# Performance work log

Hardware: AMD Instinct MI355X
Metric: run time of the kernel (lower is better)

## Reference

```python
import jax, jax.numpy as jnp
import numpy as np

B, N, D_MODEL, H, DK, DV = 2, 2048, 512, 8, 64, 64


def setup_inputs() -> dict:
    key = jax.random.key(0)
    ks = jax.random.split(key, 15)
    s = 0.02
    f = jnp.float32
    inp = {
        "x": jax.random.normal(ks[0], (B, N, D_MODEL), f),
        # frozen base projections
        "Wq": jax.random.normal(ks[1], (D_MODEL, H * DK), f) * s,
        "bq": jax.random.normal(ks[2], (H * DK,), f) * s,
        "Wk": jax.random.normal(ks[3], (D_MODEL, H * DK), f) * s,
        "bk": jax.random.normal(ks[4], (H * DK,), f) * s,
        "Wv": jax.random.normal(ks[5], (D_MODEL, H * DV), f) * s,
        "bv": jax.random.normal(ks[6], (H * DV,), f) * s,
        # 'lora' adapters (full linears in the source, added to base)
        "Wq_lora": jax.random.normal(ks[7], (D_MODEL, H * DK), f) * s,
        "bq_lora": jax.random.normal(ks[8], (H * DK,), f) * s,
        "Wk_lora": jax.random.normal(ks[9], (D_MODEL, H * DK), f) * s,
        "bk_lora": jax.random.normal(ks[10], (H * DK,), f) * s,
        "Wv_lora": jax.random.normal(ks[11], (D_MODEL, H * DV), f) * s,
        "bv_lora": jax.random.normal(ks[12], (H * DV,), f) * s,
        # output projection
        "Wo": jax.random.normal(ks[13], (H * DV, D_MODEL), f) * s,
        "bo": jax.random.normal(ks[14], (D_MODEL,), f) * s,
    }
    return inp


def reference(x, Wq, bq, Wk, bk, Wv, bv,
              Wq_lora, bq_lora, Wk_lora, bk_lora, Wv_lora, bv_lora,
              Wo, bo):
    b, n, _ = x.shape
    # base + lora pairs share the same input -> fuse into single GEMMs
    q = x @ (Wq + Wq_lora) + (bq + bq_lora)          # [b, n, H*DK]
    k = x @ (Wk + Wk_lora) + (bk + bk_lora)          # [b, n, H*DK]
    v = x @ (Wv + Wv_lora) + (bv + bv_lora)          # [b, n, H*DV]

    q = q.reshape(b, n, H, DK).transpose(0, 2, 1, 3)  # [b, H, n, DK]
    k = k.reshape(b, n, H, DK).transpose(0, 2, 1, 3)
    v = v.reshape(b, n, H, DV).transpose(0, 2, 1, 3)

    scale = 1.0 / jnp.sqrt(jnp.asarray(DK, x.dtype))
    scores = jnp.einsum('bhqd,bhkd->bhqk', q, k) * scale  # [b, H, n, n]
    att = jax.nn.softmax(scores, axis=-1)                 # attn dropout = eval identity
    out = jnp.einsum('bhqk,bhkd->bhqd', att, v)           # [b, H, n, DV]
    out = out.transpose(0, 2, 1, 3).reshape(b, n, H * DV)
    return out @ Wo + bo                                  # resid dropout = eval identity
```

## Files before the change

kernel.cpp:

```cpp
#include <hip/hip_runtime.h>
#include <hip/hip_bf16.h>

#define B_  2
#define N_  2048
#define DM_ 512
#define H_  8
#define DK_ 64
#define DV_ 64
#define BN_ (B_*N_)
#define SPLITS 2

typedef __attribute__((ext_vector_type(8))) short short8;
typedef __attribute__((ext_vector_type(4))) float f32x4;
typedef unsigned short ushort;

static __device__ __forceinline__ ushort f2bf(float x) {
    unsigned int u = __float_as_uint(x);
    unsigned int r = (u + 0x7FFFu + ((u >> 16) & 1u)) >> 16;
    return (ushort)r;
}
static __device__ __forceinline__ float bf2f(ushort u) {
    return __uint_as_float(((unsigned)u) << 16);
}
static __device__ __forceinline__ float exp2_fast(float x) {
    float r; asm("v_exp_f32 %0, %1" : "=v"(r) : "v"(x)); return r;
}
static __device__ __forceinline__ unsigned cvt_pk_bf16(float a, float b) {
    unsigned r; asm("v_cvt_pk_bf16_f32 %0, %1, %2" : "=v"(r) : "v"(a), "v"(b)); return r;
}

#define LOG2E 1.4426950408889634f

__global__ __launch_bounds__(256) void fuse_transpose4(
        const float* __restrict__ W0, const float* __restrict__ L0,
        const float* __restrict__ W1, const float* __restrict__ L1,
        const float* __restrict__ W2, const float* __restrict__ L2,
        const float* __restrict__ W3, ushort* __restrict__ WtBase) {
    const int z = blockIdx.z;
    const float* W  = (z == 0) ? W0 : (z == 1) ? W1 : (z == 2) ? W2 : W3;
    const float* WL = (z == 0) ? L0 : (z == 1) ? L1 : (z == 2) ? L2 : nullptr;
    ushort* Wt = WtBase + (size_t)z * DM_ * DM_;

    __shared__ float Ws[32][65];
    const int t  = threadIdx.x;
    const int c0 = blockIdx.x * 64;
    const int k0 = blockIdx.y * 32;
    {
        int r = t >> 4, cq = t & 15;
#pragma unroll
        for (int it = 0; it < 2; ++it) {
            int rr = r + it * 16;
            float4 v = *reinterpret_cast<const float4*>(W + (size_t)(k0 + rr) * DM_ + c0 + cq * 4);
            if (WL) {
                float4 u = *reinterpret_cast<const float4*>(WL + (size_t)(k0 + rr) * DM_ + c0 + cq * 4);
                v.x += u.x; v.y += u.y; v.z += u.z; v.w += u.w;
            }
            Ws[rr][cq * 4 + 0] = v.x; Ws[rr][cq * 4 + 1] = v.y;
            Ws[rr][cq * 4 + 2] = v.z; Ws[rr][cq * 4 + 3] = v.w;
        }
    }
    __syncthreads();
    {
        int cr = t >> 2, kq = t & 3;
        short8 o;
#pragma unroll
        for (int j = 0; j < 8; ++j) o[j] = (short)f2bf(Ws[kq * 8 + j][cr]);
        *reinterpret_cast<short8*>(Wt + (size_t)(c0 + cr) * DM_ + k0 + kq * 8) = o;
    }
}

__global__ void fuse_bias(const float* __restrict__ bq, const float* __restrict__ bqL,
                          const float* __restrict__ bk, const float* __restrict__ bkL,
                          const float* __restrict__ bv, const float* __restrict__ bvL,
                          float* __restrict__ fb) {
    int idx = blockIdx.x * blockDim.x + threadIdx.x;
    if (idx >= 3 * DM_) return;
    int w = idx >> 9, i = idx & 511;
    const float* a = (w == 0) ? bq : (w == 1) ? bk : bv;
    const float* b = (w == 0) ? bqL : (w == 1) ? bkL : bvL;
    fb[idx] = a[i] + b[i];
}

__global__ void xcast(const float* __restrict__ x, ushort* __restrict__ xb) {
    size_t idx = (size_t)blockIdx.x * blockDim.x + threadIdx.x;
    float4 v0 = *reinterpret_cast<const float4*>(x + idx * 8);
    float4 v1 = *reinterpret_cast<const float4*>(x + idx * 8 + 4);
    short8 o;
    o[0] = (short)f2bf(v0.x); o[1] = (short)f2bf(v0.y);
    o[2] = (short)f2bf(v0.z); o[3] = (short)f2bf(v0.w);
    o[4] = (short)f2bf(v1.x); o[5] = (short)f2bf(v1.y);
    o[6] = (short)f2bf(v1.z); o[7] = (short)f2bf(v1.w);
    *reinterpret_cast<short8*>(xb + idx * 8) = o;
}

template<int BN, int MODE>
__global__ __launch_bounds__(256) void gemm_bf16(const ushort* __restrict__ A,
                                                 const ushort* __restrict__ Bt,
                                                 const float* __restrict__ bias,
                                                 ushort* __restrict__ Qd,
                                                 ushort* __restrict__ Kd,
                                                 ushort* __restrict__ Vd,
                                                 float* __restrict__ outF) {
    constexpr int NWC = BN / 64;
    constexpr int NWR = 4 / NWC;
    constexpr int MI  = (128 / NWR) / 16;
    constexpr int NJ  = 4;
    const int rt = blockIdx.x, ct = blockIdx.y;
    __shared__ ushort As[128 * 64];
    __shared__ ushort Bs[BN * 64];
    const int t = threadIdx.x, lane = t & 63, w = t >> 6;
    const int wr = w / NWC, wc = w % NWC;
    const int lg = lane >> 4, lr = lane & 15;
    const int rowbase = wr * (128 / NWR);
    const int colbase = wc * 64;

    f32x4 acc[MI][NJ];
#pragma unroll
    for (int mi = 0; mi < MI; ++mi)
#pragma unroll
        for (int nj = 0; nj < NJ; ++nj) acc[mi][nj] = (f32x4){0.f, 0.f, 0.f, 0.f};

    for (int k0 = 0; k0 < DM_; k0 += 64) {
        __syncthreads();
#pragma unroll
        for (int it = 0; it < 4; ++it) {
            int cid = t + it * 256;
            int r = cid >> 3, cq = cid & 7;
            uint4 vld = *reinterpret_cast<const uint4*>(
                A + ((size_t)(rt * 128 + r)) * DM_ + k0 + cq * 8);
            *reinterpret_cast<uint4*>((char*)As + r * 128 + ((cq ^ (r & 7)) << 4)) = vld;
        }
#pragma unroll
        for (int it = 0; it < BN * 8 / 256; ++it) {
            int cid = t + it * 256;
            int r = cid >> 3, cq = cid & 7;
            uint4 vld = *reinterpret_cast<const uint4*>(
                Bt + ((size_t)(ct * BN + r)) * DM_ + k0 + cq * 8);
            *reinterpret_cast<uint4*>((char*)Bs + r * 128 + ((cq ^ (r & 7)) << 4)) = vld;
        }
        __syncthreads();
#pragma unroll
        for (int kh = 0; kh < 2; ++kh) {
            short8 a[MI], b[NJ];
#pragma unroll
            for (int mi = 0; mi < MI; ++mi) {
                int row = rowbase + mi * 16 + lr;
                a[mi] = *reinterpret_cast<const short8*>(
                    (char*)As + row * 128 + (((kh * 4 + lg) ^ (row & 7)) << 4));
            }
#pragma unroll
            for (int nj = 0; nj < NJ; ++nj) {
                int row = colbase + nj * 16 + lr;
                b[nj] = *reinterpret_cast<const short8*>(
                    (char*)Bs + row * 128 + (((kh * 4 + lg) ^ (row & 7)) << 4));
            }
#pragma unroll
            for (int mi = 0; mi < MI; ++mi)
#pragma unroll
                for (int nj = 0; nj < NJ; ++nj)
                    acc[mi][nj] = __builtin_amdgcn_mfma_f32_16x16x32_bf16(
                        a[mi], b[nj], acc[mi][nj], 0, 0, 0);
        }
    }

#pragma unroll
    for (int mi = 0; mi < MI; ++mi) {
#pragma unroll
        for (int nj = 0; nj < NJ; ++nj) {
#pragma unroll
            for (int r = 0; r < 4; ++r) {
                int m = rt * 128 + rowbase + mi * 16 + 4 * lg + r;
                int n = ct * BN + colbase + nj * 16 + lr;
                float v = acc[mi][nj][r] + bias[n];
                if (MODE == 0) {
                    int ws_ = n >> 9;
                    if (ws_ == 0) v *= 0.125f * LOG2E;
                    ushort* op = (ws_ == 0) ? Qd : (ws_ == 1) ? Kd : Vd;
                    int hd = (n >> 6) & 7, d = n & 63;
                    int bb = m >> 11, nn = m & (N_ - 1);
                    op[(((size_t)(bb * H_ + hd)) * N_ + nn) * DK_ + d] = f2bf(v);
                } else {
                    outF[(size_t)m * DM_ + n] = v;
                }
            }
        }
    }
}

__global__ __launch_bounds__(256) void vtrans(const ushort* __restrict__ Vd,
                                              ushort* __restrict__ Vt) {
    const int bh = blockIdx.y, nt = blockIdx.x;
    __shared__ ushort Ls[64 * 64];
    char* LB = (char*)Ls;
    const int t = threadIdx.x;
#pragma unroll
    for (int i = 0; i < 2; ++i) {
        int c = t + i * 256;
        int tok = c >> 3, dc = c & 7;
        uint4 v = *reinterpret_cast<const uint4*>(
            Vd + ((size_t)bh * N_ + nt * 64 + tok) * DV_ + dc * 8);
        int sw = dc ^ (tok & 7) ^ ((tok >> 3) & 7);
        *reinterpret_cast<uint4*>(LB + tok * 128 + (sw << 4)) = v;
    }
    __syncthreads();
#pragma unroll
    for (int i = 0; i < 2; ++i) {
        int c = t + i * 256;
        int d = c >> 3, tc = c & 7;
        short8 g;
#pragma unroll
        for (int j = 0; j < 8; ++j) {
            int tok = tc * 8 + j;
            int sw = (d >> 3) ^ (tok & 7) ^ ((tok >> 3) & 7);
            g[j] = *reinterpret_cast<const ushort*>(LB + tok * 128 + (sw << 4) + (d & 7) * 2);
        }
        *reinterpret_cast<short8*>(Vt + ((size_t)bh * DV_ + d) * N_ + nt * 64 + tc * 8) = g;
    }
}

__global__ __launch_bounds__(512) void attn_mfma(const ushort* __restrict__ Q,
                                                 const ushort* __restrict__ K,
                                                 const ushort* __restrict__ Vt,
                                                 ushort* __restrict__ Opart,
                                                 float2* __restrict__ Ml) {
    const int bh = blockIdx.y;
    const int qt = blockIdx.x;
    const int sp = blockIdx.z;
    const int t  = threadIdx.x;
    const int lane = t & 63;
    const int w  = t >> 6;
    const int lg = lane >> 4;
    const int lr = lane & 15;

    __shared__ ushort KsBuf[2][64 * 64];
    __shared__ ushort VtBuf[2][64 * 64];
    __shared__ ushort Ps[8][16 * 64];
    char* PsB = (char*)(Ps[w]);

    const ushort* Kb  = K  + ((size_t)bh * N_ + sp * (N_ / 2)) * DK_;
    const ushort* Vtb = Vt + (size_t)bh * DV_ * N_ + sp * (N_ / 2);

    const int srow = t >> 3, sc = t & 7;

    short8 qf[2];
    {
        const ushort* qrow = Q + ((size_t)bh * N_ + qt * 128 + w * 16 + lr) * DK_;
        qf[0] = *reinterpret_cast<const short8*>(qrow + 8 * lg);
        qf[1] = *reinterpret_cast<const short8*>(qrow + 32 + 8 * lg);
    }

    f32x4 o_[4];
#pragma unroll
    for (int i = 0; i < 4; i++) o_[i] = (f32x4){0.f, 0.f, 0.f, 0.f};
    float m1 = -1e30f, l1 = 0.f;

    uint4 kreg, vreg;
    auto issue = [&](int kt_) {
        kreg = *reinterpret_cast<const uint4*>(Kb  + ((size_t)(kt_ * 64 + srow)) * DK_ + sc * 8);
        vreg = *reinterpret_cast<const uint4*>(Vtb + (size_t)srow * N_ + kt_ * 64 + sc * 8);
    };
    auto wstage = [&](int buf_) {
        *reinterpret_cast<uint4*>((char*)(KsBuf[buf_]) + srow * 128 + ((sc ^ (srow & 7)) << 4)) = kreg;
        *reinterpret_cast<uint4*>((char*)(VtBuf[buf_]) + srow * 128 + ((sc ^ (srow & 7)) << 4)) = vreg;
    };

    issue(0);
    wstage(0);
    __syncthreads();

    const int NT = (N_ / 2) / 64;
    for (int kt = 0; kt < NT; ++kt) {
        const int cur = kt & 1;
        if (kt + 1 < NT) issue(kt + 1);

        char* KsB = (char*)(KsBuf[cur]);
        char* VtB = (char*)(VtBuf[cur]);

        f32x4 s[4];
#pragma unroll
        for (int kb = 0; kb < 4; ++kb) {
            int row = kb * 16 + lr;
            short8 k0 = *reinterpret_cast<const short8*>(
                KsB + row * 128 + ((lg ^ (row & 7)) << 4));
            short8 k1 = *reinterpret_cast<const short8*>(
                KsB + row * 128 + (((4 + lg) ^ (row & 7)) << 4));
            f32x4 z = (f32x4){0.f, 0.f, 0.f, 0.f};
            s[kb] = __builtin_amdgcn_mfma_f32_16x16x32_bf16(k0, qf[0], z, 0, 0, 0);
            s[kb] = __builtin_amdgcn_mfma_f32_16x16x32_bf16(k1, qf[1], s[kb], 0, 0, 0);
        }

        float mx = s[0][0];
#pragma unroll
        for (int kb = 0; kb < 4; ++kb)
#pragma unroll
            for (int r = 0; r < 4; ++r) mx = fmaxf(mx, s[kb][r]);
        mx = fmaxf(mx, __shfl_xor(mx, 16));
        mx = fmaxf(mx, __shfl_xor(mx, 32));

        if (!__all(mx <= m1 + 8.0f)) {
            float mnew = fmaxf(m1, mx);
            float alpha = exp2_fast(m1 - mnew);
            m1 = mnew;
            l1 *= alpha;
#pragma unroll
            for (int r = 0; r < 4; ++r) {
                float ar = __shfl(alpha, 4 * lg + r);
#pragma unroll
                for (int db = 0; db < 4; ++db) o_[db][r] *= ar;
            }
        }

        float p[4][4];
        float sum = 0.f;
#pragma unroll
        for (int kb = 0; kb < 4; ++kb)
#pragma unroll
            for (int r = 0; r < 4; ++r) { p[kb][r] = exp2_fast(s[kb][r] - m1); sum += p[kb][r]; }
        sum += __shfl_xor(sum, 16);
        sum += __shfl_xor(sum, 32);
        l1 += sum;

#pragma unroll
        for (int kb = 0; kb < 4; ++kb) {
            uint2 pk;
            pk.x = cvt_pk_bf16(p[kb][0], p[kb][1]);
            pk.y = cvt_pk_bf16(p[kb][2], p[kb][3]);
            int chunk = 2 * kb + (lg >> 1);
            *reinterpret_cast<uint2*>(
                PsB + lr * 128 + ((chunk ^ (lr & 7)) << 4) + (lg & 1) * 8) = pk;
        }

        short8 pf[2];
        {
            pf[0] = *reinterpret_cast<const short8*>(
                PsB + lr * 128 + ((lg ^ (lr & 7)) << 4));
            pf[1] = *reinterpret_cast<const short8*>(
                PsB + lr * 128 + (((4 + lg) ^ (lr & 7)) << 4));
        }
#pragma unroll
        for (int db = 0; db < 4; ++db) {
            int row = db * 16 + lr;
            short8 v0 = *reinterpret_cast<const short8*>(
                VtB + row * 128 + ((lg ^ (row & 7)) << 4));
            short8 v1 = *reinterpret_cast<const short8*>(
                VtB + row * 128 + (((4 + lg) ^ (row & 7)) << 4));
            o_[db] = __builtin_amdgcn_mfma_f32_16x16x32_bf16(pf[0], v0, o_[db], 0, 0, 0);
            o_[db] = __builtin_amdgcn_mfma_f32_16x16x32_bf16(pf[1], v1, o_[db], 0, 0, 0);
        }

        if (kt + 1 < NT) wstage(cur ^ 1);
        __syncthreads();
    }

    const size_t rowbase = ((size_t)(sp * 16 + bh)) * N_ + qt * 128 + w * 16;
#pragma unroll
    for (int r = 0; r < 4; ++r) {
        int n_loc = 4 * lg + r;
#pragma unroll
        for (int db = 0; db < 4; ++db) {
            Opart[(rowbase + n_loc) * DV_ + db * 16 + lr] = f2bf(o_[db][r]);
        }
    }
    if (lg == 0) {
        Ml[rowbase + lr] = make_float2(m1, l1);
    }
}

__global__ __launch_bounds__(256) void merge_splits(const ushort* __restrict__ Opart,
                                                    const float2* __restrict__ Ml,
                                                    ushort* __restrict__ Od) {
    int gid = blockIdx.x * 256 + threadIdx.x;
    int row = gid >> 4;
    int dv  = (gid & 15) * 4;
    const int R = 16 * N_;
    float2 ml0 = Ml[row];
    float2 ml1 = Ml[R + row];
    float M  = fmaxf(ml0.x, ml1.x);
    float w0 = exp2_fast(ml0.x - M);
    float w1 = exp2_fast(ml1.x - M);
    float inv = 1.f / (w0 * ml0.y + w1 * ml1.y);
    uint2 a = *reinterpret_cast<const uint2*>(Opart + (size_t)row * DV_ + dv);
    uint2 b = *reinterpret_cast<const uint2*>(Opart + ((size_t)R + row) * DV_ + dv);
    const ushort* ae = reinterpret_cast<const ushort*>(&a);
    const ushort* be = reinterpret_cast<const ushort*>(&b);
    uint2 o;
    unsigned* oe = reinterpret_cast<unsigned*>(&o);
#pragma unroll
    for (int half = 0; half < 2; ++half) {
        float v0 = (w0 * bf2f(ae[half * 2 + 0]) + w1 * bf2f(be[half * 2 + 0])) * inv;
        float v1 = (w0 * bf2f(ae[half * 2 + 1]) + w1 * bf2f(be[half * 2 + 1])) * inv;
        oe[half] = cvt_pk_bf16(v0, v1);
    }
    int bh = row >> 11, n = row & (N_ - 1);
    int bb = bh >> 3, h = bh & 7;
    *reinterpret_cast<uint2*>(Od + ((size_t)(bb * N_ + n)) * (H_ * DV_) + h * DV_ + dv) = o;
}

extern "C" void kernel_launch(void* const* d_in, const int* in_sizes, int n_in,
                              void* d_out, int out_size, void* d_ws, size_t ws_size,
                              hipStream_t stream) {
    const float* x   = (const float*)d_in[0];
    const float* Wq  = (const float*)d_in[1];
    const float* bq  = (const float*)d_in[2];
    const float* Wk  = (const float*)d_in[3];
    const float* bk  = (const float*)d_in[4];
    const float* Wv  = (const float*)d_in[5];
    const float* bv  = (const float*)d_in[6];
    const float* WqL = (const float*)d_in[7];
    const float* bqL = (const float*)d_in[8];
    const float* WkL = (const float*)d_in[9];
    const float* bkL = (const float*)d_in[10];
    const float* WvL = (const float*)d_in[11];
    const float* bvL = (const float*)d_in[12];
    const float* Wo  = (const float*)d_in[13];
    const float* bo  = (const float*)d_in[14];

    ushort* Wt_all = (ushort*)d_ws;
    ushort* Wot    = Wt_all + (size_t)3 * DM_ * DM_;
    float*  fb     = (float*)(Wt_all + (size_t)4 * DM_ * DM_);
    ushort* xbf    = (ushort*)(fb + 3 * DM_);
    ushort* Qd     = xbf + (size_t)BN_ * DM_;
    ushort* Kd     = Qd + (size_t)B_ * H_ * N_ * DK_;
    ushort* Vd     = Kd + (size_t)B_ * H_ * N_ * DK_;
    ushort* Vtd    = Vd + (size_t)B_ * H_ * N_ * DV_;
    ushort* Od     = Vtd + (size_t)B_ * H_ * N_ * DV_;
    ushort* Opart  = Od + (size_t)B_ * H_ * N_ * DV_;
    float2* Ml     = (float2*)(Opart + (size_t)SPLITS * B_ * H_ * N_ * DV_);

    float* out = (float*)d_out;

    fuse_transpose4<<<dim3(8, 16, 4), 256, 0, stream>>>(Wq, WqL, Wk, WkL, Wv, WvL, Wo, Wt_all);
    fuse_bias<<<6, 256, 0, stream>>>(bq, bqL, bk, bkL, bv, bvL, fb);
    xcast<<<1024, 256, 0, stream>>>(x, xbf);

    gemm_bf16<128, 0><<<dim3(32, 12), 256, 0, stream>>>(xbf, Wt_all, fb, Qd, Kd, Vd, nullptr);
    vtrans<<<dim3(32, 16), 256, 0, stream>>>(Vd, Vtd);
    attn_mfma<<<dim3(16, 16, SPLITS), 512, 0, stream>>>(Qd, Kd, Vtd, Opart, Ml);
    merge_splits<<<(B_ * H_ * N_ * 16) / 256, 256, 0, stream>>>(Opart, Ml, Od);
    gemm_bf16<64, 1><<<dim3(32, 8), 256, 0, stream>>>(Od, Wot, bo, nullptr, nullptr, nullptr, out);
}
```

Before: 72.08 us.

## Double-buffer GEMM shared-memory staging and merge xcast with bias fusion

The bf16 GEMM now prefetches the next K-tile from global memory into registers while running the MFMAs on the current tile, then writes it into a second LDS buffer. This cuts one barrier per iteration and hides global load latency. The cost is doubled LDS use and extra registers, which may lower occupancy. Separately, the x cast and the bias fusion now run in one kernel, saving a launch.

New measurement: 103.6 us. 1.44x slower.

```diff
diff --git a/kernel.cpp b/kernel.cpp
--- a/kernel.cpp
+++ b/kernel.cpp
@@ -69,28 +69,31 @@
     }
 }
 
-__global__ void fuse_bias(const float* __restrict__ bq, const float* __restrict__ bqL,
-                          const float* __restrict__ bk, const float* __restrict__ bkL,
-                          const float* __restrict__ bv, const float* __restrict__ bvL,
-                          float* __restrict__ fb) {
-    int idx = blockIdx.x * blockDim.x + threadIdx.x;
-    if (idx >= 3 * DM_) return;
-    int w = idx >> 9, i = idx & 511;
-    const float* a = (w == 0) ? bq : (w == 1) ? bk : bv;
-    const float* b = (w == 0) ? bqL : (w == 1) ? bkL : bvL;
-    fb[idx] = a[i] + b[i];
-}
-
-__global__ void xcast(const float* __restrict__ x, ushort* __restrict__ xb) {
-    size_t idx = (size_t)blockIdx.x * blockDim.x + threadIdx.x;
-    float4 v0 = *reinterpret_cast<const float4*>(x + idx * 8);
-    float4 v1 = *reinterpret_cast<const float4*>(x + idx * 8 + 4);
-    short8 o;
-    o[0] = (short)f2bf(v0.x); o[1] = (short)f2bf(v0.y);
-    o[2] = (short)f2bf(v0.z); o[3] = (short)f2bf(v0.w);
-    o[4] = (short)f2bf(v1.x); o[5] = (short)f2bf(v1.y);
-    o[6] = (short)f2bf(v1.z); o[7] = (short)f2bf(v1.w);
-    *reinterpret_cast<short8*>(xb + idx * 8) = o;
+__global__ void xcast_bias(const float* __restrict__ x, ushort* __restrict__ xb,
+                           const float* __restrict__ bq, const float* __restrict__ bqL,
+                           const float* __restrict__ bk, const float* __restrict__ bkL,
+                           const float* __restrict__ bv, const float* __restrict__ bvL,
+                           float* __restrict__ fb) {
+    const int bid = blockIdx.x;
+    if (bid < 1024) {
+        size_t idx = (size_t)bid * blockDim.x + threadIdx.x;
+        float4 v0 = *reinterpret_cast<const float4*>(x + idx * 8);
+        float4 v1 = *reinterpret_cast<const float4*>(x + idx * 8 + 4);
+        short8 o;
+        o[0] = (short)f2bf(v0.x); o[1] = (short)f2bf(v0.y);
+        o[2] = (short)f2bf(v0.z); o[3] = (short)f2bf(v0.w);
+        o[4] = (short)f2bf(v1.x); o[5] = (short)f2bf(v1.y);
+        o[6] = (short)f2bf(v1.z); o[7] = (short)f2bf(v1.w);
+        *reinterpret_cast<short8*>(xb + idx * 8) = o;
+    } else {
+        int idx = (bid - 1024) * 256 + threadIdx.x;
+        if (idx < 3 * DM_) {
+            int w = idx >> 9, i = idx & 511;
+            const float* a = (w == 0) ? bq : (w == 1) ? bk : bv;
+            const float* b = (w == 0) ? bqL : (w == 1) ? bkL : bvL;
+            fb[idx] = a[i] + b[i];
+        }
+    }
 }
 
 template<int BN, int MODE>
@@ -105,14 +108,16 @@
     constexpr int NWR = 4 / NWC;
     constexpr int MI  = (128 / NWR) / 16;
     constexpr int NJ  = 4;
+    constexpr int BIT = BN * 8 / 256;
     const int rt = blockIdx.x, ct = blockIdx.y;
-    __shared__ ushort As[128 * 64];
-    __shared__ ushort Bs[BN * 64];
+    __shared__ ushort As[2][128 * 64];
+    __shared__ ushort Bs[2][BN * 64];
     const int t = threadIdx.x, lane = t & 63, w = t >> 6;
     const int wr = w / NWC, wc = w % NWC;
     const int lg = lane >> 4, lr = lane & 15;
     const int rowbase = wr * (128 / NWR);
     const int colbase = wc * 64;
+    const int sr = t >> 3, scq = t & 7;
 
     f32x4 acc[MI][NJ];
 #pragma unroll
@@ -120,25 +125,43 @@
 #pragma unroll
         for (int nj = 0; nj < NJ; ++nj) acc[mi][nj] = (f32x4){0.f, 0.f, 0.f, 0.f};
 
+    uint4 aReg[4], bReg[BIT];
+    auto issue = [&](int k0) {
+#pragma unroll
+        for (int it = 0; it < 4; ++it) {
+            int r = sr + it * 32;
+            aReg[it] = *reinterpret_cast<const uint4*>(
+                A + ((size_t)(rt * 128 + r)) * DM_ + k0 + scq * 8);
+        }
+#pragma unroll
+        for (int it = 0; it < BIT; ++it) {
+            int r = sr + it * 32;
+            bReg[it] = *reinterpret_cast<const uint4*>(
+                Bt + ((size_t)(ct * BN + r)) * DM_ + k0 + scq * 8);
+        }
+    };
+    auto wstage = [&](int buf) {
+#pragma unroll
+        for (int it = 0; it < 4; ++it) {
+            int r = sr + it * 32;
+            *reinterpret_cast<uint4*>(
+                (char*)(As[buf]) + r * 128 + ((scq ^ (r & 7)) << 4)) = aReg[it];
+        }
+#pragma unroll
+        for (int it = 0; it < BIT; ++it) {
+            int r = sr + it * 32;
+            *reinterpret_cast<uint4*>(
+                (char*)(Bs[buf]) + r * 128 + ((scq ^ (r & 7)) << 4)) = bReg[it];
+        }
+    };
+
+    issue(0);
+    wstage(0);
+    __syncthreads();
+
     for (int k0 = 0; k0 < DM_; k0 += 64) {
-        __syncthreads();
-#pragma unroll
-        for (int it = 0; it < 4; ++it) {
-            int cid = t + it * 256;
-            int r = cid >> 3, cq = cid & 7;
-            uint4 vld = *reinterpret_cast<const uint4*>(
-                A + ((size_t)(rt * 128 + r)) * DM_ + k0 + cq * 8);
-            *reinterpret_cast<uint4*>((char*)As + r * 128 + ((cq ^ (r & 7)) << 4)) = vld;
-        }
-#pragma unroll
-        for (int it = 0; it < BN * 8 / 256; ++it) {
-            int cid = t + it * 256;
-            int r = cid >> 3, cq = cid & 7;
-            uint4 vld = *reinterpret_cast<const uint4*>(
-                Bt + ((size_t)(ct * BN + r)) * DM_ + k0 + cq * 8);
-            *reinterpret_cast<uint4*>((char*)Bs + r * 128 + ((cq ^ (r & 7)) << 4)) = vld;
-        }
-        __syncthreads();
+        const int cur = (k0 >> 6) & 1;
+        if (k0 + 64 < DM_) issue(k0 + 64);
 #pragma unroll
         for (int kh = 0; kh < 2; ++kh) {
             short8 a[MI], b[NJ];
@@ -146,13 +169,13 @@
             for (int mi = 0; mi < MI; ++mi) {
                 int row = rowbase + mi * 16 + lr;
                 a[mi] = *reinterpret_cast<const short8*>(
-                    (char*)As + row * 128 + (((kh * 4 + lg) ^ (row & 7)) << 4));
+                    (char*)(As[cur]) + row * 128 + (((kh * 4 + lg) ^ (row & 7)) << 4));
             }
 #pragma unroll
             for (int nj = 0; nj < NJ; ++nj) {
                 int row = colbase + nj * 16 + lr;
                 b[nj] = *reinterpret_cast<const short8*>(
-                    (char*)Bs + row * 128 + (((kh * 4 + lg) ^ (row & 7)) << 4));
+                    (char*)(Bs[cur]) + row * 128 + (((kh * 4 + lg) ^ (row & 7)) << 4));
             }
 #pragma unroll
             for (int mi = 0; mi < MI; ++mi)
@@ -161,6 +184,8 @@
                     acc[mi][nj] = __builtin_amdgcn_mfma_f32_16x16x32_bf16(
                         a[mi], b[nj], acc[mi][nj], 0, 0, 0);
         }
+        if (k0 + 64 < DM_) wstage(cur ^ 1);
+        __syncthreads();
     }
 
 #pragma unroll
@@ -430,8 +455,7 @@
     float* out = (float*)d_out;
 
     fuse_transpose4<<<dim3(8, 16, 4), 256, 0, stream>>>(Wq, WqL, Wk, WkL, Wv, WvL, Wo, Wt_all);
-    fuse_bias<<<6, 256, 0, stream>>>(bq, bqL, bk, bkL, bv, bvL, fb);
-    xcast<<<1024, 256, 0, stream>>>(x, xbf);
+    xcast_bias<<<1030, 256, 0, stream>>>(x, xbf, bq, bqL, bk, bkL, bv, bvL, fb);
 
     gemm_bf16<128, 0><<<dim3(32, 12), 256, 0, stream>>>(xbf, Wt_all, fb, Qd, Kd, Vd, nullptr);
     vtrans<<<dim3(32, 16), 256, 0, stream>>>(Vd, Vtd);
```
